# Performance work log

Measured on AMD Instinct MI355X. Metric: run time of the kernel, lower is better.

Reference implementation:

```python
import jax, jax.numpy as jnp
import numpy as np

N_EMBD = 2048
N_HEAD = 32
N_KV_HEAD = 8
HEAD_DIM = N_EMBD // N_HEAD  # 64
N_REP = N_HEAD // N_KV_HEAD  # 4
WINDOW = 1024
ROPE_BASE = 10000.0


def setup_inputs() -> dict:
    key = jax.random.key(0)
    ks = jax.random.split(key, 4)
    B, T = 2, 4096
    x = jax.random.normal(ks[0], (B, T, N_EMBD), dtype=jnp.float32)
    s = 0.02
    Wq = jax.random.normal(ks[1], (N_EMBD, N_HEAD * HEAD_DIM), dtype=jnp.float32) * s
    Wkv = jax.random.normal(ks[2], (N_EMBD, 2 * N_KV_HEAD * HEAD_DIM), dtype=jnp.float32) * s
    Wo = jax.random.normal(ks[3], (N_EMBD, N_EMBD), dtype=jnp.float32) * s
    return {"x": x, "Wq": Wq, "Wkv": Wkv, "Wo": Wo}


def _rotate_half(x):
    x1, x2 = jnp.split(x, 2, axis=-1)
    return jnp.concatenate([-x2, x1], axis=-1)


def _rope_cos_sin(T, dtype):
    inv_freq = 1.0 / (ROPE_BASE ** (jnp.arange(0, HEAD_DIM, 2, dtype=jnp.float32) / HEAD_DIM))
    t = jnp.arange(T, dtype=jnp.float32)
    freqs = jnp.einsum("i,j->ij", t, inv_freq)  # [T, HEAD_DIM/2]
    emb = jnp.concatenate([freqs, freqs], axis=-1)  # [T, HEAD_DIM]
    return jnp.cos(emb).astype(dtype)[None, None], jnp.sin(emb).astype(dtype)[None, None]


def reference(x, Wq, Wkv, Wo):
    B, T, _ = x.shape
    q = (x @ Wq).reshape(B, T, N_HEAD, HEAD_DIM).transpose(0, 2, 1, 3)  # [B,H,T,D]
    kv = (x @ Wkv).reshape(B, T, 2, N_KV_HEAD, HEAD_DIM)
    k = kv[:, :, 0].transpose(0, 2, 1, 3)  # [B,KV,T,D]
    v = kv[:, :, 1].transpose(0, 2, 1, 3)

    cos, sin = _rope_cos_sin(T, x.dtype)
    q = q * cos + _rotate_half(q) * sin
    k = k * cos + _rotate_half(k) * sin

    # repeat kv heads for GQA: [B,KV,T,D] -> [B,H,T,D]
    k = jnp.repeat(k, N_REP, axis=1)
    v = jnp.repeat(v, N_REP, axis=1)

    scale = 1.0 / jnp.sqrt(jnp.asarray(HEAD_DIM, dtype=x.dtype))
    scores = jnp.einsum("bhqd,bhkd->bhqk", q, k) * scale  # [B,H,T,T]

    # causal + sliding window mask: attend iff q - window < kpos <= qpos
    qpos = jnp.arange(T)[:, None]
    kpos = jnp.arange(T)[None, :]
    allowed = (kpos <= qpos) & (kpos > qpos - WINDOW)
    scores = jnp.where(allowed[None, None], scores, jnp.asarray(-jnp.inf, dtype=scores.dtype))

    attn = jax.nn.softmax(scores, axis=-1)
    out = jnp.einsum("bhqk,bhkd->bhqd", attn, v)  # [B,H,T,D]
    out = out.transpose(0, 2, 1, 3).reshape(B, T, N_EMBD)
    return out @ Wo
```

## Files before the change

kernel.cpp:

```cpp
#include <hip/hip_runtime.h>
#include <cstddef>

typedef unsigned short ushort_t;
typedef unsigned int uint32;

typedef __bf16   bf16x8 __attribute__((ext_vector_type(8)));
typedef __bf16   bf16x2 __attribute__((ext_vector_type(2)));
typedef __bf16   bf16x4 __attribute__((ext_vector_type(4)));
typedef float    f32x16 __attribute__((ext_vector_type(16)));
typedef float    f32x4  __attribute__((ext_vector_type(4)));
typedef ushort_t u16x8  __attribute__((ext_vector_type(8)));
typedef ushort_t u16x4  __attribute__((ext_vector_type(4)));
typedef uint32   u32x4  __attribute__((ext_vector_type(4)));
typedef uint32   u32x2  __attribute__((ext_vector_type(2)));

__device__ __forceinline__ ushort_t f2b(float f) {
  uint32 u = __builtin_bit_cast(uint32, f);
  u += 0x7fff + ((u >> 16) & 1);
  return (ushort_t)(u >> 16);
}

__device__ __forceinline__ f32x16 mfma32(bf16x8 a, bf16x8 b, f32x16 c) {
  return __builtin_amdgcn_mfma_f32_32x32x16_bf16(a, b, c, 0, 0, 0);
}

__device__ __forceinline__ void gload_lds16(const void* g, void* l) {
  __builtin_amdgcn_global_load_lds((const __attribute__((address_space(1))) void*)g,
                                   (__attribute__((address_space(3))) void*)l, 16, 0, 0);
}

__launch_bounds__(256)
__global__ void k_rope_table(float* __restrict__ cosT, float* __restrict__ sinT) {
  int idx = blockIdx.x * 256 + threadIdx.x;
  int t = idx >> 5, j = idx & 31;
  float invf = __expf(-(float)j * (9.210340371976184f / 32.0f));
  float ang = (float)t * invf;
  cosT[idx] = cosf(ang);
  sinT[idx] = sinf(ang);
}

__launch_bounds__(256)
__global__ void k_cvt_x(const float* __restrict__ in, ushort_t* __restrict__ out) {
  size_t i = ((size_t)blockIdx.x * 256 + threadIdx.x) * 8;
  f32x4 a = *(const f32x4*)(in + i);
  f32x4 b = *(const f32x4*)(in + i + 4);
  u16x8 v = {f2b(a[0]), f2b(a[1]), f2b(a[2]), f2b(a[3]),
             f2b(b[0]), f2b(b[1]), f2b(b[2]), f2b(b[3])};
  *(u16x8*)(out + i) = v;
}

__launch_bounds__(256)
__global__ void k_transpose(const float* __restrict__ W, ushort_t* __restrict__ Wt,
                            int K, int N) {
  __shared__ __align__(16) ushort_t tile[64][72];
  int nbx = N >> 6;
  int bx = blockIdx.x % nbx, by = blockIdx.x / nbx;
  int r0 = by << 6, c0 = bx << 6;
  int tid = threadIdx.x;
#pragma unroll
  for (int p = 0; p < 2; p++) {
    int id = p * 256 + tid;
    int r = id >> 3, cs = id & 7;
    const float* src = W + (size_t)(r0 + r) * N + c0 + cs * 8;
    f32x4 a = *(const f32x4*)(src);
    f32x4 b = *(const f32x4*)(src + 4);
    u16x8 v = {f2b(a[0]), f2b(a[1]), f2b(a[2]), f2b(a[3]),
               f2b(b[0]), f2b(b[1]), f2b(b[2]), f2b(b[3])};
    *(u16x8*)&tile[r][cs * 8] = v;
  }
  __syncthreads();
#pragma unroll
  for (int p = 0; p < 2; p++) {
    int id = p * 256 + tid;
    int oc = id >> 3, ocs = id & 7;
    u16x8 v;
#pragma unroll
    for (int j = 0; j < 8; j++) v[j] = tile[ocs * 8 + j][oc];
    *(u16x8*)(Wt + (size_t)(c0 + oc) * K + r0 + ocs * 8) = v;
  }
}

template <int MODE>
__launch_bounds__(256)
__global__ void k_gemm(const ushort_t* __restrict__ A, const ushort_t* __restrict__ Bt,
                       int M, int N, int K,
                       ushort_t* __restrict__ out0, float* __restrict__ outf,
                       ushort_t* __restrict__ kout, ushort_t* __restrict__ vout,
                       const float* __restrict__ cosT, const float* __restrict__ sinT) {
  __shared__ __align__(16) ushort_t lds[2][2][128 * 32];
  const int tid = threadIdx.x;
  const int wave = tid >> 6, lane = tid & 63;
  const int l31 = lane & 31, hf = lane >> 5;
  const int nTn = N >> 7;
  const int bm = blockIdx.x / nTn, bn = blockIdx.x % nTn;
  const int row0 = bm << 7, col0 = bn << 7;

  f32x16 acc[2][2] = {};

  auto stage = [&](int buf, int k0) {
#pragma unroll
    for (int side = 0; side < 2; side++) {
      const ushort_t* src = side ? Bt : A;
      int r0g = side ? col0 : row0;
#pragma unroll
      for (int i = 0; i < 2; i++) {
        int rl = wave * 32 + i * 16 + (lane >> 2);
        int cs = lane & 3;
        const ushort_t* gp = src + (size_t)(r0g + rl) * K + k0 + cs * 8;
        ushort_t* lp = &lds[buf][side][(wave * 32 + i * 16) * 32];
        gload_lds16(gp, lp);
      }
    }
  };

  stage(0, 0);
  __syncthreads();

  const int wm = wave >> 1, wn = wave & 1;
  const int nk = K >> 5;
  for (int kt = 0; kt < nk; kt++) {
    const int buf = kt & 1;
    if (kt + 1 < nk) stage(buf ^ 1, (kt + 1) << 5);
    const ushort_t* la = &lds[buf][0][0];
    const ushort_t* lb = &lds[buf][1][0];
#pragma unroll
    for (int ks = 0; ks < 2; ks++) {
      const int kc = ks * 2 + hf;
      bf16x8 af[2], bg[2];
#pragma unroll
      for (int mi = 0; mi < 2; mi++) {
        int r = wm * 64 + mi * 32 + l31;
        af[mi] = *(const bf16x8*)(la + r * 32 + kc * 8);
      }
#pragma unroll
      for (int ni = 0; ni < 2; ni++) {
        int r = wn * 64 + ni * 32 + l31;
        bg[ni] = *(const bf16x8*)(lb + r * 32 + kc * 8);
      }
#pragma unroll
      for (int mi = 0; mi < 2; mi++)
#pragma unroll
        for (int ni = 0; ni < 2; ni++)
          acc[mi][ni] = mfma32(af[mi], bg[ni], acc[mi][ni]);
    }
    __syncthreads();
  }

  if (MODE == 0) {
#pragma unroll
    for (int mi = 0; mi < 2; mi++)
#pragma unroll
      for (int ni = 0; ni < 2; ni++) {
        int cg = col0 + wn * 64 + ni * 32 + l31;
#pragma unroll
        for (int r = 0; r < 16; r++) {
          int rg = row0 + wm * 64 + mi * 32 + (r & 3) + 8 * (r >> 2) + 4 * hf;
          outf[(size_t)rg * N + cg] = acc[mi][ni][r];
        }
      }
  } else if (MODE == 1) {
    int cg = col0 + wn * 64 + l31;
#pragma unroll
    for (int mi = 0; mi < 2; mi++)
#pragma unroll
      for (int r = 0; r < 16; r++) {
        int rg = row0 + wm * 64 + mi * 32 + (r & 3) + 8 * (r >> 2) + 4 * hf;
        int t = rg & 4095;
        float c = cosT[t * 32 + l31];
        float s = sinT[t * 32 + l31];
        float lo = acc[mi][0][r], hi = acc[mi][1][r];
        out0[(size_t)rg * N + cg]      = f2b(lo * c - hi * s);
        out0[(size_t)rg * N + cg + 32] = f2b(hi * c + lo * s);
      }
  } else {
    int cb = col0 + wn * 64;
    if (cb < 512) {
      int g = cb >> 6;
#pragma unroll
      for (int mi = 0; mi < 2; mi++)
#pragma unroll
        for (int r = 0; r < 16; r++) {
          int rg = row0 + wm * 64 + mi * 32 + (r & 3) + 8 * (r >> 2) + 4 * hf;
          int t = rg & 4095, b = rg >> 12;
          float c = cosT[t * 32 + l31];
          float s = sinT[t * 32 + l31];
          float lo = acc[mi][0][r], hi = acc[mi][1][r];
          size_t base = ((size_t)(b * 8 + g) * 4096 + t) * 64;
          kout[base + l31]      = f2b(lo * c - hi * s);
          kout[base + l31 + 32] = f2b(hi * c + lo * s);
        }
    } else {
#pragma unroll
      for (int mi = 0; mi < 2; mi++)
#pragma unroll
        for (int ni = 0; ni < 2; ni++) {
          int vd = cb + ni * 32 + l31 - 512;
          int g = vd >> 6, d = vd & 63;
#pragma unroll
          for (int g2 = 0; g2 < 4; g2++) {
            int rg = row0 + wm * 64 + mi * 32 + 8 * g2 + 4 * hf;
            int b = rg >> 12, tl = rg & 4095;
            u16x4 pk = {f2b(acc[mi][ni][g2 * 4 + 0]), f2b(acc[mi][ni][g2 * 4 + 1]),
                        f2b(acc[mi][ni][g2 * 4 + 2]), f2b(acc[mi][ni][g2 * 4 + 3])};
            size_t base = (((size_t)(b * 8 + g) * 128 + (tl >> 5)) * 64 + d) * 32;
            *(u16x4*)(vout + base + (tl & 31)) = pk;
          }
        }
    }
  }
}

__launch_bounds__(256)
__global__ void k_attn(ushort_t* __restrict__ q, const ushort_t* __restrict__ kk,
                       const ushort_t* __restrict__ vT) {
  __shared__ __align__(16) ushort_t Kl[2][32][68];
  __shared__ __align__(16) ushort_t Vl[2][64][36];
  const int tid = threadIdx.x;
  const int wave = tid >> 6, lane = tid & 63;
  const int l31 = lane & 31, hf = lane >> 5;
  const int chunk = gridDim.x >> 3;
  const int blk = ((int)blockIdx.x & 7) * chunk + ((int)blockIdx.x >> 3);
  const int bh = blk >> 5, qt4 = 31 - (blk & 31);
  const int b = bh >> 5, hd = bh & 31;
  const int g = hd >> 2;
  const int qt = qt4 * 4 + wave;
  const int t0 = qt << 5;
  const float NEG = -1e30f;
  const float C = 0.18033688011112042f;

  const ushort_t* qp = q + ((size_t)(b * 4096 + t0 + l31)) * 2048 + hd * 64 + hf * 8;
  bf16x8 qf[4];
#pragma unroll
  for (int ks = 0; ks < 4; ks++) qf[ks] = *(const bf16x8*)(qp + ks * 16);

  const ushort_t* kg = kk + (size_t)(b * 8 + g) * 4096 * 64;
  const ushort_t* vg = vT + (size_t)(b * 8 + g) * 128 * 64 * 32;

  f32x16 o[2] = {};
  float m_i = -60.f, l_i = 0.f;

  const int KT0 = (qt4 >= 8) ? ((qt4 * 128 - 1023) >> 5) : 0;
  const int KTmax = qt4 * 4 + 3;

  const int krow = tid >> 3, kchk = tid & 7;
  const int vrow = tid >> 2, vchk = tid & 3;

  {
    u32x4 kv = *(const u32x4*)(kg + ((size_t)(KT0 << 5) + krow) * 64 + kchk * 8);
    u32x4 vv = *(const u32x4*)(vg + (size_t)KT0 * 2048 + vrow * 32 + vchk * 8);
    *(u32x2*)&Kl[0][krow][kchk * 8]     = (u32x2){kv[0], kv[1]};
    *(u32x2*)&Kl[0][krow][kchk * 8 + 4] = (u32x2){kv[2], kv[3]};
    *(u32x2*)&Vl[0][vrow][vchk * 8]     = (u32x2){vv[0], vv[1]};
    *(u32x2*)&Vl[0][vrow][vchk * 8 + 4] = (u32x2){vv[2], vv[3]};
  }
  __syncthreads();

  for (int kt = KT0; kt <= KTmax; kt++) {
    const int buf = (kt - KT0) & 1;
    const int kb = kt << 5;
    const bool more = (kt < KTmax);

    u32x4 kv, vv;
    if (more) {
      kv = *(const u32x4*)(kg + ((size_t)(kb + 32) + krow) * 64 + kchk * 8);
      vv = *(const u32x4*)(vg + (size_t)(kt + 1) * 2048 + vrow * 32 + vchk * 8);
    }

    const bool live = (kt <= qt) && (kb > t0 - 1055);
    if (live) {
      bf16x8 kf[4];
#pragma unroll
      for (int ks = 0; ks < 4; ks++) {
        u32x2 a0 = *(const u32x2*)&Kl[buf][l31][hf * 8 + ks * 16];
        u32x2 a1 = *(const u32x2*)&Kl[buf][l31][hf * 8 + ks * 16 + 4];
        u32x4 w = {a0[0], a0[1], a1[0], a1[1]};
        kf[ks] = __builtin_bit_cast(bf16x8, w);
      }
      f32x16 sa = {};
      __builtin_amdgcn_s_setprio(1);
#pragma unroll
      for (int ks = 0; ks < 4; ks++) sa = mfma32(kf[ks], qf[ks], sa);
      __builtin_amdgcn_s_setprio(0);

      bf16x8 vf[2][2];
#pragma unroll
      for (int ks = 0; ks < 2; ks++)
#pragma unroll
        for (int mi = 0; mi < 2; mi++) {
          u32x2 a0 = *(const u32x2*)&Vl[buf][mi * 32 + l31][hf * 8 + ks * 16];
          u32x2 a1 = *(const u32x2*)&Vl[buf][mi * 32 + l31][hf * 8 + ks * 16 + 4];
          u32x4 w = {a0[0], a0[1], a1[0], a1[1]};
          vf[ks][mi] = __builtin_bit_cast(bf16x8, w);
        }

      const bool need_mask = (kt == qt) || (kb < t0 - 992);
      if (need_mask) {
        int base = (t0 + l31) - kb - 4 * hf;
#pragma unroll
        for (int r = 0; r < 16; r++) {
          int off = (r & 3) + 8 * (r >> 2);
          sa[r] = ((unsigned)(base - off) < 1024u) ? sa[r] : NEG;
        }
      }
      float t0m = fmaxf(fmaxf(sa[0], sa[1]), sa[2]);
      float t1m = fmaxf(fmaxf(sa[3], sa[4]), sa[5]);
      float t2m = fmaxf(fmaxf(sa[6], sa[7]), sa[8]);
      float t3m = fmaxf(fmaxf(sa[9], sa[10]), sa[11]);
      float t4m = fmaxf(fmaxf(sa[12], sa[13]), sa[14]);
      float mx = fmaxf(fmaxf(fmaxf(t0m, t1m), t2m), fmaxf(fmaxf(t3m, t4m), sa[15]));
      mx = fmaxf(mx, __shfl_xor(mx, 32, 64));
      float mx2 = mx * C;
      if (!__all(mx2 - m_i <= 8.f)) {
        float m_new = fmaxf(m_i, mx2);
        float alpha = __builtin_amdgcn_exp2f(m_i - m_new);
        l_i *= alpha;
#pragma unroll
        for (int r = 0; r < 16; r++) { o[0][r] *= alpha; o[1][r] *= alpha; }
        m_i = m_new;
      }
      float p[16];
#pragma unroll
      for (int r = 0; r < 16; r++)
        p[r] = __builtin_amdgcn_exp2f(__builtin_fmaf(sa[r], C, -m_i));
      float ps = (((p[0] + p[1]) + (p[2] + p[3])) + ((p[4] + p[5]) + (p[6] + p[7]))) +
                 (((p[8] + p[9]) + (p[10] + p[11])) + ((p[12] + p[13]) + (p[14] + p[15])));
      ps += __shfl_xor(ps, 32, 64);
      l_i += ps;

      uint32 u[8];
#pragma unroll
      for (int i = 0; i < 8; i++) {
        bf16x2 t2 = {(__bf16)p[2 * i], (__bf16)p[2 * i + 1]};
        u[i] = __builtin_bit_cast(uint32, t2);
      }

#pragma unroll
      for (int ks = 0; ks < 2; ks++) {
        uint32 own0 = hf ? u[4 * ks + 2] : u[4 * ks + 0];
        uint32 own1 = hf ? u[4 * ks + 3] : u[4 * ks + 1];
        uint32 snd0 = hf ? u[4 * ks + 0] : u[4 * ks + 2];
        uint32 snd1 = hf ? u[4 * ks + 1] : u[4 * ks + 3];
        uint32 r0 = (uint32)__shfl_xor((int)snd0, 32, 64);
        uint32 r1 = (uint32)__shfl_xor((int)snd1, 32, 64);
        u32x4 fr;
        fr[0] = hf ? r0 : own0;
        fr[1] = hf ? r1 : own1;
        fr[2] = hf ? own0 : r0;
        fr[3] = hf ? own1 : r1;
        bf16x8 pf = __builtin_bit_cast(bf16x8, fr);
        __builtin_amdgcn_s_setprio(1);
        o[0] = mfma32(vf[ks][0], pf, o[0]);
        o[1] = mfma32(vf[ks][1], pf, o[1]);
        __builtin_amdgcn_s_setprio(0);
      }
    }

    if (more) {
      *(u32x2*)&Kl[buf ^ 1][krow][kchk * 8]     = (u32x2){kv[0], kv[1]};
      *(u32x2*)&Kl[buf ^ 1][krow][kchk * 8 + 4] = (u32x2){kv[2], kv[3]};
      *(u32x2*)&Vl[buf ^ 1][vrow][vchk * 8]     = (u32x2){vv[0], vv[1]};
      *(u32x2*)&Vl[buf ^ 1][vrow][vchk * 8 + 4] = (u32x2){vv[2], vv[3]};
    }
    __syncthreads();
  }

  float inv_l = 1.0f / fmaxf(l_i, 1e-20f);
  ushort_t* op = q + ((size_t)(b * 4096 + t0 + l31)) * 2048 + hd * 64;
#pragma unroll
  for (int mi = 0; mi < 2; mi++)
#pragma unroll
    for (int g2 = 0; g2 < 4; g2++) {
      int d0 = mi * 32 + 8 * g2 + 4 * hf;
      bf16x4 pk = {(__bf16)(o[mi][g2 * 4 + 0] * inv_l), (__bf16)(o[mi][g2 * 4 + 1] * inv_l),
                   (__bf16)(o[mi][g2 * 4 + 2] * inv_l), (__bf16)(o[mi][g2 * 4 + 3] * inv_l)};
      *(bf16x4*)(op + d0) = pk;
    }
}

extern "C" void kernel_launch(void* const* d_in, const int* in_sizes, int n_in,
                              void* d_out, int out_size, void* d_ws, size_t ws_size,
                              hipStream_t stream) {
  const float* x   = (const float*)d_in[0];
  const float* Wq  = (const float*)d_in[1];
  const float* Wkv = (const float*)d_in[2];
  const float* Wo  = (const float*)d_in[3];
  float* outp = (float*)d_out;

  const int BT = in_sizes[0] / 2048;
  const int Bb = BT / 4096;

  char* ob = (char*)d_out;
  const size_t MB = 1024 * 1024;
  ushort_t* x_c  = (ushort_t*)(ob);
  ushort_t* WqT  = (ushort_t*)(ob + 32 * MB);
  ushort_t* WkvT = (ushort_t*)(ob + 40 * MB);
  ushort_t* kbuf = (ushort_t*)(ob + 44 * MB);
  ushort_t* vbuf = (ushort_t*)(ob + 52 * MB);
  float*    cosT = (float*)   (ob + 60 * MB);
  float*    sinT = (float*)   (ob + 60 * MB + 512 * 1024);

  char* ws = (char*)d_ws;
  ushort_t* qbuf = (ushort_t*)(ws);
  ushort_t* WoT  = (ushort_t*)(ws + 32 * MB);

  k_rope_table<<<512, 256, 0, stream>>>(cosT, sinT);
  k_cvt_x<<<BT * 2048 / (256 * 8), 256, 0, stream>>>(x, x_c);
  k_transpose<<<32 * 32, 256, 0, stream>>>(Wq, WqT, 2048, 2048);
  k_transpose<<<32 * 16, 256, 0, stream>>>(Wkv, WkvT, 2048, 1024);
  k_transpose<<<32 * 32, 256, 0, stream>>>(Wo, WoT, 2048, 2048);

  k_gemm<1><<<(BT / 128) * (2048 / 128), 256, 0, stream>>>(
      x_c, WqT, BT, 2048, 2048, qbuf, nullptr, nullptr, nullptr, cosT, sinT);
  k_gemm<2><<<(BT / 128) * (1024 / 128), 256, 0, stream>>>(
      x_c, WkvT, BT, 1024, 2048, nullptr, nullptr, kbuf, vbuf, cosT, sinT);

  k_attn<<<Bb * 32 * 32, 256, 0, stream>>>(qbuf, kbuf, vbuf);

  k_gemm<0><<<(BT / 128) * (2048 / 128), 256, 0, stream>>>(
      qbuf, WoT, BT, 2048, 2048, nullptr, outp, nullptr, nullptr, nullptr, nullptr);
}
```

Before: 528.5 us.

## Merge prep kernels into one launch and remap GEMM blocks for L2 locality

Merges the rope table, x conversion, and three weight-transpose kernels into a single k_prep launch that dispatches on block index, so four kernel launches go away and the independent prep work can run concurrently. The GEMM block index is also remapped: blocks are strided across 8 groups (likely meant to match the XCD round-robin dispatch) and then grouped into 4x4 supertiles so co-resident blocks share A and B tiles in cache. The remap assumes the grid size is divisible by 8 and nTn by 4, which holds for these shapes.

```diff
diff --git a/kernel.cpp b/kernel.cpp
--- a/kernel.cpp
+++ b/kernel.cpp
@@ -30,33 +30,44 @@
 }
 
 __launch_bounds__(256)
-__global__ void k_rope_table(float* __restrict__ cosT, float* __restrict__ sinT) {
-  int idx = blockIdx.x * 256 + threadIdx.x;
-  int t = idx >> 5, j = idx & 31;
-  float invf = __expf(-(float)j * (9.210340371976184f / 32.0f));
-  float ang = (float)t * invf;
-  cosT[idx] = cosf(ang);
-  sinT[idx] = sinf(ang);
-}
-
-__launch_bounds__(256)
-__global__ void k_cvt_x(const float* __restrict__ in, ushort_t* __restrict__ out) {
-  size_t i = ((size_t)blockIdx.x * 256 + threadIdx.x) * 8;
-  f32x4 a = *(const f32x4*)(in + i);
-  f32x4 b = *(const f32x4*)(in + i + 4);
-  u16x8 v = {f2b(a[0]), f2b(a[1]), f2b(a[2]), f2b(a[3]),
-             f2b(b[0]), f2b(b[1]), f2b(b[2]), f2b(b[3])};
-  *(u16x8*)(out + i) = v;
-}
-
-__launch_bounds__(256)
-__global__ void k_transpose(const float* __restrict__ W, ushort_t* __restrict__ Wt,
-                            int K, int N) {
+__global__ void k_prep(const float* __restrict__ x, ushort_t* __restrict__ x_c, int nCvt,
+                       const float* __restrict__ Wq, ushort_t* __restrict__ WqT,
+                       const float* __restrict__ Wkv, ushort_t* __restrict__ WkvT,
+                       const float* __restrict__ Wo, ushort_t* __restrict__ WoT,
+                       float* __restrict__ cosT, float* __restrict__ sinT) {
   __shared__ __align__(16) ushort_t tile[64][72];
+  const int tid = threadIdx.x;
+  int bid = blockIdx.x;
+  if (bid < 512) {
+    int idx = bid * 256 + tid;
+    int t = idx >> 5, j = idx & 31;
+    float invf = __expf(-(float)j * (9.210340371976184f / 32.0f));
+    float ang = (float)t * invf;
+    cosT[idx] = cosf(ang);
+    sinT[idx] = sinf(ang);
+    return;
+  }
+  bid -= 512;
+  if (bid < nCvt) {
+    size_t i = ((size_t)bid * 256 + tid) * 8;
+    f32x4 a = *(const f32x4*)(x + i);
+    f32x4 b = *(const f32x4*)(x + i + 4);
+    u16x8 v = {f2b(a[0]), f2b(a[1]), f2b(a[2]), f2b(a[3]),
+               f2b(b[0]), f2b(b[1]), f2b(b[2]), f2b(b[3])};
+    *(u16x8*)(x_c + i) = v;
+    return;
+  }
+  bid -= nCvt;
+  const float* W;
+  ushort_t* Wt;
+  int N;
+  if (bid < 1024)      { W = Wq;  Wt = WqT;  N = 2048; }
+  else if (bid < 1536) { W = Wkv; Wt = WkvT; N = 1024; bid -= 1024; }
+  else                 { W = Wo;  Wt = WoT;  N = 2048; bid -= 1536; }
+  const int K = 2048;
   int nbx = N >> 6;
-  int bx = blockIdx.x % nbx, by = blockIdx.x / nbx;
+  int bx = bid % nbx, by = bid / nbx;
   int r0 = by << 6, c0 = bx << 6;
-  int tid = threadIdx.x;
 #pragma unroll
   for (int p = 0; p < 2; p++) {
     int id = p * 256 + tid;
@@ -92,7 +103,12 @@
   const int wave = tid >> 6, lane = tid & 63;
   const int l31 = lane & 31, hf = lane >> 5;
   const int nTn = N >> 7;
-  const int bm = blockIdx.x / nTn, bn = blockIdx.x % nTn;
+  const int bid = (int)blockIdx.x;
+  const int blk = ((bid & 7) * (int)(gridDim.x >> 3)) + (bid >> 3);
+  const int st = blk >> 4, si = blk & 15;
+  const int nStc = nTn >> 2;
+  const int stm = st / nStc, stn = st % nStc;
+  const int bm = stm * 4 + (si >> 2), bn = stn * 4 + (si & 3);
   const int row0 = bm << 7, col0 = bn << 7;
 
   f32x16 acc[2][2] = {};
@@ -403,11 +419,9 @@
   ushort_t* qbuf = (ushort_t*)(ws);
   ushort_t* WoT  = (ushort_t*)(ws + 32 * MB);
 
-  k_rope_table<<<512, 256, 0, stream>>>(cosT, sinT);
-  k_cvt_x<<<BT * 2048 / (256 * 8), 256, 0, stream>>>(x, x_c);
-  k_transpose<<<32 * 32, 256, 0, stream>>>(Wq, WqT, 2048, 2048);
-  k_transpose<<<32 * 16, 256, 0, stream>>>(Wkv, WkvT, 2048, 1024);
-  k_transpose<<<32 * 32, 256, 0, stream>>>(Wo, WoT, 2048, 2048);
+  const int nCvt = BT;
+  k_prep<<<512 + nCvt + 2560, 256, 0, stream>>>(x, x_c, nCvt, Wq, WqT, Wkv, WkvT,
+                                                Wo, WoT, cosT, sinT);
 
   k_gemm<1><<<(BT / 128) * (2048 / 128), 256, 0, stream>>>(
       x_c, WqT, BT, 2048, 2048, qbuf, nullptr, nullptr, nullptr, cosT, sinT);
```

After: 510.1 us. 3.5% less time.
